# Performance work log

Hardware: AMD Instinct MI355X
Metric: run time of the kernel (lower is better)

Reference implementation:

```python
import jax, jax.numpy as jnp
import numpy as np
from jax import lax

S = 9      # patch feature size (3x3 flattened)
HID = 15   # MI-net hidden width
B = 4096
IMG = 192
PAD = 6


def _linear_params(k, fin, fout):
    bound = 1.0 / np.sqrt(fin)
    kw, kb = jax.random.split(k)
    w = jax.random.uniform(kw, (fout, fin), minval=-bound, maxval=bound, dtype=jnp.float32)
    b = jax.random.uniform(kb, (fout,), minval=-bound, maxval=bound, dtype=jnp.float32)
    return w, b


def setup_inputs() -> dict:
    key = jax.random.key(0)
    ks = jax.random.split(key, 12)
    x = jax.random.normal(ks[0], (B, 1, IMG, IMG), dtype=jnp.float32)
    hc = IMG // 3  # conv output side (stride-3 valid conv)
    ij = jax.random.randint(ks[1], (B, 2), 0, hc, dtype=jnp.int32)
    perm = jax.random.permutation(ks[2], B).astype(jnp.int32)
    cb = 1.0 / np.sqrt(1 * 3 * 3)
    conv_w = jax.random.uniform(ks[3], (1, 1, 3, 3), minval=-cb, maxval=cb, dtype=jnp.float32)
    conv_b = jax.random.uniform(ks[4], (1,), minval=-cb, maxval=cb, dtype=jnp.float32)
    xw1, xb1 = _linear_params(ks[5], S, S)
    xw2, xb2 = _linear_params(ks[6], S, S)
    xw3, xb3 = _linear_params(ks[7], S, HID)
    yw1, yb1 = _linear_params(ks[8], S, S)
    yw2, yb2 = _linear_params(ks[9], S, S)
    yw3, yb3 = _linear_params(ks[10], S, HID)
    fw, fb = _linear_params(ks[11], HID, 1)
    return dict(x=x, ij=ij, perm=perm, conv_w=conv_w, conv_b=conv_b,
                xw1=xw1, xb1=xb1, xw2=xw2, xb2=xb2, xw3=xw3, xb3=xb3,
                yw1=yw1, yb1=yb1, yw2=yw2, yb2=yb2, yw3=yw3, yb3=yb3,
                fw=fw, fb=fb)


def _mi_net(p1, p2, xw1, xb1, xw2, xb2, xw3, xb3,
            yw1, yb1, yw2, yb2, yw3, yb3, fw, fb):
    ix = p1 + jax.nn.relu(p1 @ xw1.T + xb1)
    ix = ix + jax.nn.relu(ix @ xw2.T + xb2)
    ix = ix @ xw3.T + xb3
    iy = p2 + jax.nn.relu(p2 @ yw1.T + yb1)
    iy = iy + jax.nn.relu(iy @ yw2.T + yb2)
    iy = iy @ yw3.T + yb3
    h1 = jax.nn.relu(ix + iy)
    return h1 @ fw.T + fb  # [B, 1]


def reference(x, ij, perm, conv_w, conv_b,
              xw1, xb1, xw2, xb2, xw3, xb3,
              yw1, yb1, yw2, yb2, yw3, yb3, fw, fb):
    # stride-3 valid conv: [B,1,IMG,IMG] -> [B,1,64,64]
    co = lax.conv_general_dilated(x, conv_w, (3, 3), 'VALID',
                                  dimension_numbers=('NCHW', 'OIHW', 'NCHW'))
    co = co[:, 0] + conv_b[0]  # [B, Hc, Wc]
    bn, hc, wc = co.shape
    # pad_circular(data, 6)[i:i+3, j:j+6] == data[(i-6+r) % Hc, (j-6+c) % Wc]
    rows = (ij[:, 0:1] - PAD + jnp.arange(3, dtype=jnp.int32)) % hc  # [B,3]
    cols = (ij[:, 1:2] - PAD + jnp.arange(6, dtype=jnp.int32)) % wc  # [B,6]
    rect = co[jnp.arange(bn)[:, None, None], rows[:, :, None], cols[:, None, :]]  # [B,3,6]
    patch1 = rect[:, :, :3].reshape(-1, S)
    patch2 = rect[:, :, 3:].reshape(-1, S)
    patch2_sh = patch2[perm]
    pred_xy = _mi_net(patch1, patch2, xw1, xb1, xw2, xb2, xw3, xb3,
                      yw1, yb1, yw2, yb2, yw3, yb3, fw, fb)
    pred_x_y = _mi_net(patch1, patch2_sh, xw1, xb1, xw2, xb2, xw3, xb3,
                       yw1, yb1, yw2, yb2, yw3, yb3, fw, fb)
    ret = jnp.mean(pred_xy) - jnp.log(jnp.mean(jnp.exp(pred_x_y)))
    return -ret
```

## Files before the change

kernel.cpp:

```cpp
#include <hip/hip_runtime.h>
#include <math.h>

#define BATCH 4096
#define IMGD 192
#define HC 64
#define PADV 6
#define NBLK2 256
#define IPB 16

__device__ __forceinline__ void branch9(const float* __restrict__ s, int off,
                                        const float* __restrict__ p, float* __restrict__ out)
{
    float v[9];
    #pragma unroll
    for (int j = 0; j < 9; ++j) {
        float a = s[off + 81 + j];
        #pragma unroll
        for (int k = 0; k < 9; ++k) a += p[k] * s[off + j * 9 + k];
        v[j] = p[j] + fmaxf(a, 0.0f);
    }
    float u[9];
    #pragma unroll
    for (int j = 0; j < 9; ++j) {
        float a = s[off + 171 + j];
        #pragma unroll
        for (int k = 0; k < 9; ++k) a += v[k] * s[off + 90 + j * 9 + k];
        u[j] = v[j] + fmaxf(a, 0.0f);
    }
    #pragma unroll
    for (int j = 0; j < 15; ++j) {
        float a = s[off + 315 + j];
        #pragma unroll
        for (int k = 0; k < 9; ++k) a += u[k] * s[off + 180 + j * 9 + k];
        out[j] = a;
    }
}

__global__ __launch_bounds__(256) void k_fused(
    const float* __restrict__ x, const int* __restrict__ ij,
    const int* __restrict__ perm,
    const float* __restrict__ cw, const float* __restrict__ cb,
    const float* __restrict__ xw1, const float* __restrict__ xb1,
    const float* __restrict__ xw2, const float* __restrict__ xb2,
    const float* __restrict__ xw3, const float* __restrict__ xb3,
    const float* __restrict__ yw1, const float* __restrict__ yb1,
    const float* __restrict__ yw2, const float* __restrict__ yb2,
    const float* __restrict__ yw3, const float* __restrict__ yb3,
    const float* __restrict__ fw, const float* __restrict__ fb,
    float* __restrict__ partials)
{
    __shared__ float s[676];
    __shared__ int   pidx[IPB];
    __shared__ int   ij4[IPB * 4];
    __shared__ float lpatch[IPB * 27];
    __shared__ float bout[48 * 15];

    int t  = threadIdx.x;
    int b0 = blockIdx.x * IPB;

    for (int i = t; i < 81; i += 256)  { s[i] = xw1[i];        s[330 + i] = yw1[i];
                                         s[90 + i] = xw2[i];   s[420 + i] = yw2[i]; }
    for (int i = t; i < 135; i += 256) { s[180 + i] = xw3[i];  s[510 + i] = yw3[i]; }
    if (t < 9)  { s[81 + t] = xb1[t];   s[171 + t] = xb2[t];
                  s[411 + t] = yb1[t];  s[501 + t] = yb2[t]; }
    if (t < 15) { s[315 + t] = xb3[t];  s[645 + t] = yb3[t];  s[660 + t] = fw[t]; }
    if (t == 0) s[675] = fb[0];

    float w[9];
    #pragma unroll
    for (int i = 0; i < 9; ++i) w[i] = cw[i];
    float cbias = cb[0];

    if (t < IPB) pidx[t] = perm[b0 + t];
    __syncthreads();
    if (t < 2 * IPB) {
        int item = t & (IPB - 1);
        int sel  = t >> 4;
        int bb   = sel ? pidx[item] : (b0 + item);
        ij4[item * 4 + sel * 2 + 0] = ij[2 * bb];
        ij4[item * 4 + sel * 2 + 1] = ij[2 * bb + 1];
    }
    __syncthreads();

    for (int idx = t; idx < IPB * 27; idx += 256) {
        int item = idx / 27;
        int p    = idx - item * 27;
        int r, c, sel, slot;
        if (p < 18) {
            r = p / 6;  c = p - r * 6;  sel = 0;
            int half = (c >= 3) ? 1 : 0;
            slot = half * 9 + r * 3 + (c - 3 * half);
        } else {
            int q = p - 18;
            r = q / 3;  c = 3 + (q - r * 3);  sel = 1;
            slot = 18 + q;
        }
        int bb = sel ? pidx[item] : (b0 + item);
        int i0 = ij4[item * 4 + sel * 2], j0 = ij4[item * 4 + sel * 2 + 1];
        int rr = i0 - PADV + r;  if (rr < 0) rr += HC;
        int cc = j0 - PADV + c;  if (cc < 0) cc += HC;
        const float* xp = x + (size_t)bb * (IMGD * IMGD)
                            + (size_t)(rr * 3) * IMGD + cc * 3;
        float v = cbias;
        v += xp[0]          * w[0] + xp[1]            * w[1] + xp[2]            * w[2];
        v += xp[IMGD]       * w[3] + xp[IMGD + 1]     * w[4] + xp[IMGD + 2]     * w[5];
        v += xp[2 * IMGD]   * w[6] + xp[2 * IMGD + 1] * w[7] + xp[2 * IMGD + 2] * w[8];
        lpatch[item * 27 + slot] = v;
    }
    __syncthreads();

    if (t < 48) {
        int item   = t & 15;
        int branch = t >> 4;
        int woff   = (branch == 0) ? 0 : 330;
        int pbase  = item * 27 + branch * 9;
        float p[9];
        #pragma unroll
        for (int k = 0; k < 9; ++k) p[k] = lpatch[pbase + k];
        float o[15];
        branch9(s, woff, p, o);
        #pragma unroll
        for (int j = 0; j < 15; ++j) bout[t * 15 + j] = o[j];
    }
    __syncthreads();

    if (t < IPB) {
        float fbv = s[675];
        float pxy = fbv, pxs = fbv;
        #pragma unroll
        for (int j = 0; j < 15; ++j) {
            float oxj  = bout[t * 15 + j];
            float oyj  = bout[(16 + t) * 15 + j];
            float oysj = bout[(32 + t) * 15 + j];
            float fwj  = s[660 + j];
            pxy += fmaxf(oxj + oyj,  0.0f) * fwj;
            pxs += fmaxf(oxj + oysj, 0.0f) * fwj;
        }
        float e = expf(pxs);
        #pragma unroll
        for (int o = 8; o > 0; o >>= 1) {
            pxy += __shfl_down(pxy, o);
            e   += __shfl_down(e, o);
        }
        if (t == 0) {
            partials[blockIdx.x]         = pxy;
            partials[NBLK2 + blockIdx.x] = e;
        }
    }
}

__global__ __launch_bounds__(256) void k_final(const float* __restrict__ partials,
                                               float* __restrict__ out)
{
    __shared__ float r1[4], r2[4];
    int t = threadIdx.x;
    float sx = partials[t];
    float se = partials[NBLK2 + t];
    #pragma unroll
    for (int o = 32; o > 0; o >>= 1) {
        sx += __shfl_down(sx, o);
        se += __shfl_down(se, o);
    }
    int wid = t >> 6, lane = t & 63;
    if (lane == 0) { r1[wid] = sx; r2[wid] = se; }
    __syncthreads();
    if (t == 0) {
        float S  = (r1[0] + r1[1]) + (r1[2] + r1[3]);
        float E  = (r2[0] + r2[1]) + (r2[2] + r2[3]);
        out[0] = logf(E / (float)BATCH) - S / (float)BATCH;
    }
}

extern "C" void kernel_launch(void* const* d_in, const int* in_sizes, int n_in,
                              void* d_out, int out_size, void* d_ws, size_t ws_size,
                              hipStream_t stream)
{
    const float* x    = (const float*)d_in[0];
    const int*   ij   = (const int*)d_in[1];
    const int*   perm = (const int*)d_in[2];
    const float* cw   = (const float*)d_in[3];
    const float* cb   = (const float*)d_in[4];
    const float* xw1  = (const float*)d_in[5];
    const float* xb1  = (const float*)d_in[6];
    const float* xw2  = (const float*)d_in[7];
    const float* xb2  = (const float*)d_in[8];
    const float* xw3  = (const float*)d_in[9];
    const float* xb3  = (const float*)d_in[10];
    const float* yw1  = (const float*)d_in[11];
    const float* yb1  = (const float*)d_in[12];
    const float* yw2  = (const float*)d_in[13];
    const float* yb2  = (const float*)d_in[14];
    const float* yw3  = (const float*)d_in[15];
    const float* yb3  = (const float*)d_in[16];
    const float* fw   = (const float*)d_in[17];
    const float* fb   = (const float*)d_in[18];

    float* partials = (float*)d_ws;

    k_fused<<<NBLK2, 256, 0, stream>>>(x, ij, perm, cw, cb,
                                       xw1, xb1, xw2, xb2, xw3, xb3,
                                       yw1, yb1, yw2, yb2, yw3, yb3,
                                       fw, fb, partials);
    k_final<<<1, 256, 0, stream>>>(partials, (float*)d_out);
}
```

Before: 12.38 us.

## Bulk-load ij table to LDS, remove a barrier, unroll gathers, pad weights for vector loads

Each block now copies the whole 32 KB ij table into shared memory with int4 loads, at the same time as the perm and weight loads, which removes one barrier and the dependent ij gather round trip. The conv gather loop is unrolled into two fixed slots per thread so all 18 global loads are issued before any arithmetic. Weight rows are padded to 12 floats so the MLP can read them with float4 shared loads. The MLP threads are spread across three wavefronts instead of packed into one. The cost is 32 KB of extra LDS per block and redundant global reads of ij by all 256 blocks, which may reduce occupancy.

New measurement: 12.73 us. +2.8%, slower.

```diff
diff --git a/kernel.cpp b/kernel.cpp
--- a/kernel.cpp
+++ b/kernel.cpp
@@ -8,33 +8,16 @@
 #define NBLK2 256
 #define IPB 16
 
-__device__ __forceinline__ void branch9(const float* __restrict__ s, int off,
-                                        const float* __restrict__ p, float* __restrict__ out)
-{
-    float v[9];
-    #pragma unroll
-    for (int j = 0; j < 9; ++j) {
-        float a = s[off + 81 + j];
-        #pragma unroll
-        for (int k = 0; k < 9; ++k) a += p[k] * s[off + j * 9 + k];
-        v[j] = p[j] + fmaxf(a, 0.0f);
-    }
-    float u[9];
-    #pragma unroll
-    for (int j = 0; j < 9; ++j) {
-        float a = s[off + 171 + j];
-        #pragma unroll
-        for (int k = 0; k < 9; ++k) a += v[k] * s[off + 90 + j * 9 + k];
-        u[j] = v[j] + fmaxf(a, 0.0f);
-    }
-    #pragma unroll
-    for (int j = 0; j < 15; ++j) {
-        float a = s[off + 315 + j];
-        #pragma unroll
-        for (int k = 0; k < 9; ++k) a += u[k] * s[off + 180 + j * 9 + k];
-        out[j] = a;
-    }
-}
+#define XB 0
+#define YB 432
+#define W1O 0
+#define W2O 108
+#define W3O 216
+#define B1O 396
+#define B2O 405
+#define B3O 414
+#define FWO 864
+#define FBO 879
 
 __global__ __launch_bounds__(256) void k_fused(
     const float* __restrict__ x, const int* __restrict__ ij,
@@ -49,90 +32,153 @@
     const float* __restrict__ fw, const float* __restrict__ fb,
     float* __restrict__ partials)
 {
-    __shared__ float s[676];
+    __shared__ __align__(16) float s[880];
+    __shared__ __align__(16) int   ija[BATCH * 2];
     __shared__ int   pidx[IPB];
-    __shared__ int   ij4[IPB * 4];
     __shared__ float lpatch[IPB * 27];
     __shared__ float bout[48 * 15];
 
     int t  = threadIdx.x;
     int b0 = blockIdx.x * IPB;
 
-    for (int i = t; i < 81; i += 256)  { s[i] = xw1[i];        s[330 + i] = yw1[i];
-                                         s[90 + i] = xw2[i];   s[420 + i] = yw2[i]; }
-    for (int i = t; i < 135; i += 256) { s[180 + i] = xw3[i];  s[510 + i] = yw3[i]; }
-    if (t < 9)  { s[81 + t] = xb1[t];   s[171 + t] = xb2[t];
-                  s[411 + t] = yb1[t];  s[501 + t] = yb2[t]; }
-    if (t < 15) { s[315 + t] = xb3[t];  s[645 + t] = yb3[t];  s[660 + t] = fw[t]; }
-    if (t == 0) s[675] = fb[0];
+    {
+        int4* d = (int4*)ija;
+        const int4* g = (const int4*)ij;
+        #pragma unroll
+        for (int i = 0; i < 8; ++i) d[t + 256 * i] = g[t + 256 * i];
+    }
+    if (t < IPB) pidx[t] = perm[b0 + t];
+
+    for (int i = t; i < 108; i += 256) {
+        int row = i / 12, col = i - row * 12;
+        if (col < 9) {
+            int src = row * 9 + col;
+            s[XB + W1O + i] = xw1[src];  s[XB + W2O + i] = xw2[src];
+            s[YB + W1O + i] = yw1[src];  s[YB + W2O + i] = yw2[src];
+        }
+    }
+    for (int i = t; i < 180; i += 256) {
+        int row = i / 12, col = i - row * 12;
+        if (col < 9) {
+            int src = row * 9 + col;
+            s[XB + W3O + i] = xw3[src];  s[YB + W3O + i] = yw3[src];
+        }
+    }
+    if (t >= 192) {
+        int tb = t - 192;
+        if (tb < 9)       { s[XB + B1O + tb] = xb1[tb];  s[XB + B2O + tb] = xb2[tb];
+                            s[YB + B1O + tb] = yb1[tb];  s[YB + B2O + tb] = yb2[tb]; }
+        else if (tb < 24) { int j = tb - 9;  s[XB + B3O + j] = xb3[j];  s[YB + B3O + j] = yb3[j]; }
+        else if (tb < 39) { int j = tb - 24; s[FWO + j] = fw[j]; }
+        else if (tb == 39){ s[FBO] = fb[0]; }
+    }
 
     float w[9];
     #pragma unroll
     for (int i = 0; i < 9; ++i) w[i] = cw[i];
     float cbias = cb[0];
-
-    if (t < IPB) pidx[t] = perm[b0 + t];
-    __syncthreads();
-    if (t < 2 * IPB) {
-        int item = t & (IPB - 1);
-        int sel  = t >> 4;
-        int bb   = sel ? pidx[item] : (b0 + item);
-        ij4[item * 4 + sel * 2 + 0] = ij[2 * bb];
-        ij4[item * 4 + sel * 2 + 1] = ij[2 * bb + 1];
-    }
-    __syncthreads();
-
-    for (int idx = t; idx < IPB * 27; idx += 256) {
-        int item = idx / 27;
-        int p    = idx - item * 27;
-        int r, c, sel, slot;
-        if (p < 18) {
-            r = p / 6;  c = p - r * 6;  sel = 0;
-            int half = (c >= 3) ? 1 : 0;
-            slot = half * 9 + r * 3 + (c - 3 * half);
-        } else {
-            int q = p - 18;
-            r = q / 3;  c = 3 + (q - r * 3);  sel = 1;
-            slot = 18 + q;
-        }
-        int bb = sel ? pidx[item] : (b0 + item);
-        int i0 = ij4[item * 4 + sel * 2], j0 = ij4[item * 4 + sel * 2 + 1];
-        int rr = i0 - PADV + r;  if (rr < 0) rr += HC;
-        int cc = j0 - PADV + c;  if (cc < 0) cc += HC;
-        const float* xp = x + (size_t)bb * (IMGD * IMGD)
-                            + (size_t)(rr * 3) * IMGD + cc * 3;
-        float v = cbias;
-        v += xp[0]          * w[0] + xp[1]            * w[1] + xp[2]            * w[2];
-        v += xp[IMGD]       * w[3] + xp[IMGD + 1]     * w[4] + xp[IMGD + 2]     * w[5];
-        v += xp[2 * IMGD]   * w[6] + xp[2 * IMGD + 1] * w[7] + xp[2 * IMGD + 2] * w[8];
-        lpatch[item * 27 + slot] = v;
-    }
-    __syncthreads();
-
-    if (t < 48) {
-        int item   = t & 15;
-        int branch = t >> 4;
-        int woff   = (branch == 0) ? 0 : 330;
-        int pbase  = item * 27 + branch * 9;
-        float p[9];
-        #pragma unroll
-        for (int k = 0; k < 9; ++k) p[k] = lpatch[pbase + k];
-        float o[15];
-        branch9(s, woff, p, o);
-        #pragma unroll
-        for (int j = 0; j < 15; ++j) bout[t * 15 + j] = o[j];
+    __syncthreads();
+
+    {
+        int idxA = t;
+        int itemA = idxA / 27;  int pA = idxA - itemA * 27;
+        int rA, cA, selA, slotA;
+        if (pA < 18) { rA = pA / 6; cA = pA - rA * 6; selA = 0;
+                       int h = (cA >= 3); slotA = h * 9 + rA * 3 + (cA - 3 * h); }
+        else         { int q = pA - 18; rA = q / 3; cA = 3 + q - rA * 3; selA = 1; slotA = 18 + q; }
+        int bbA = selA ? pidx[itemA] : (b0 + itemA);
+        int i0A = ija[2 * bbA], j0A = ija[2 * bbA + 1];
+        int rrA = i0A - PADV + rA;  if (rrA < 0) rrA += HC;
+        int ccA = j0A - PADV + cA;  if (ccA < 0) ccA += HC;
+        const float* pa = x + (size_t)bbA * (IMGD * IMGD) + (size_t)(rrA * 3) * IMGD + ccA * 3;
+
+        bool hasB = (t < 176);
+        int idxB = t + 256;
+        int itemB = idxB / 27;  int pB = idxB - itemB * 27;
+        int rB, cB, selB, slotB;
+        if (pB < 18) { rB = pB / 6; cB = pB - rB * 6; selB = 0;
+                       int h = (cB >= 3); slotB = h * 9 + rB * 3 + (cB - 3 * h); }
+        else         { int q = pB - 18; rB = q / 3; cB = 3 + q - rB * 3; selB = 1; slotB = 18 + q; }
+        itemB = hasB ? itemB : 0;
+        int bbB = selB ? pidx[itemB] : (b0 + itemB);
+        int i0B = ija[2 * bbB], j0B = ija[2 * bbB + 1];
+        int rrB = i0B - PADV + rB;  if (rrB < 0) rrB += HC;
+        int ccB = j0B - PADV + cB;  if (ccB < 0) ccB += HC;
+        const float* pb = hasB ? (x + (size_t)bbB * (IMGD * IMGD) + (size_t)(rrB * 3) * IMGD + ccB * 3)
+                               : pa;
+
+        float a0 = pa[0],          a1 = pa[1],            a2 = pa[2];
+        float a3 = pa[IMGD],       a4 = pa[IMGD + 1],     a5 = pa[IMGD + 2];
+        float a6 = pa[2 * IMGD],   a7 = pa[2 * IMGD + 1], a8 = pa[2 * IMGD + 2];
+        float e0 = pb[0],          e1 = pb[1],            e2 = pb[2];
+        float e3 = pb[IMGD],       e4 = pb[IMGD + 1],     e5 = pb[IMGD + 2];
+        float e6 = pb[2 * IMGD],   e7 = pb[2 * IMGD + 1], e8 = pb[2 * IMGD + 2];
+
+        float vA = cbias + a0*w[0] + a1*w[1] + a2*w[2] + a3*w[3] + a4*w[4]
+                         + a5*w[5] + a6*w[6] + a7*w[7] + a8*w[8];
+        lpatch[itemA * 27 + slotA] = vA;
+        if (hasB) {
+            float vB = cbias + e0*w[0] + e1*w[1] + e2*w[2] + e3*w[3] + e4*w[4]
+                             + e5*w[5] + e6*w[6] + e7*w[7] + e8*w[8];
+            lpatch[itemB * 27 + slotB] = vB;
+        }
+    }
+    __syncthreads();
+
+    {
+        int wv = t >> 6, l = t & 63;
+        if (wv < 3 && l < 16) {
+            int woff = (wv == 0) ? XB : YB;
+            int ib = wv * 16 + l;
+            float p[9];
+            #pragma unroll
+            for (int k = 0; k < 9; ++k) p[k] = lpatch[l * 27 + wv * 9 + k];
+
+            float v[9];
+            #pragma unroll
+            for (int j = 0; j < 9; ++j) {
+                const float4 r0 = *(const float4*)&s[woff + W1O + j * 12];
+                const float4 r1 = *(const float4*)&s[woff + W1O + j * 12 + 4];
+                float acc = s[woff + B1O + j]
+                    + r0.x*p[0] + r0.y*p[1] + r0.z*p[2] + r0.w*p[3]
+                    + r1.x*p[4] + r1.y*p[5] + r1.z*p[6] + r1.w*p[7]
+                    + s[woff + W1O + j * 12 + 8] * p[8];
+                v[j] = p[j] + fmaxf(acc, 0.0f);
+            }
+            float u[9];
+            #pragma unroll
+            for (int j = 0; j < 9; ++j) {
+                const float4 r0 = *(const float4*)&s[woff + W2O + j * 12];
+                const float4 r1 = *(const float4*)&s[woff + W2O + j * 12 + 4];
+                float acc = s[woff + B2O + j]
+                    + r0.x*v[0] + r0.y*v[1] + r0.z*v[2] + r0.w*v[3]
+                    + r1.x*v[4] + r1.y*v[5] + r1.z*v[6] + r1.w*v[7]
+                    + s[woff + W2O + j * 12 + 8] * v[8];
+                u[j] = v[j] + fmaxf(acc, 0.0f);
+            }
+            #pragma unroll
+            for (int j = 0; j < 15; ++j) {
+                const float4 r0 = *(const float4*)&s[woff + W3O + j * 12];
+                const float4 r1 = *(const float4*)&s[woff + W3O + j * 12 + 4];
+                float acc = s[woff + B3O + j]
+                    + r0.x*u[0] + r0.y*u[1] + r0.z*u[2] + r0.w*u[3]
+                    + r1.x*u[4] + r1.y*u[5] + r1.z*u[6] + r1.w*u[7]
+                    + s[woff + W3O + j * 12 + 8] * u[8];
+                bout[ib * 15 + j] = acc;
+            }
+        }
     }
     __syncthreads();
 
     if (t < IPB) {
-        float fbv = s[675];
+        float fbv = s[FBO];
         float pxy = fbv, pxs = fbv;
         #pragma unroll
         for (int j = 0; j < 15; ++j) {
             float oxj  = bout[t * 15 + j];
             float oyj  = bout[(16 + t) * 15 + j];
             float oysj = bout[(32 + t) * 15 + j];
-            float fwj  = s[660 + j];
+            float fwj  = s[FWO + j];
             pxy += fmaxf(oxj + oyj,  0.0f) * fwj;
             pxs += fmaxf(oxj + oysj, 0.0f) * fwj;
         }
@@ -165,8 +211,8 @@
     if (lane == 0) { r1[wid] = sx; r2[wid] = se; }
     __syncthreads();
     if (t == 0) {
-        float S  = (r1[0] + r1[1]) + (r1[2] + r1[3]);
-        float E  = (r2[0] + r2[1]) + (r2[2] + r2[3]);
+        float S = (r1[0] + r1[1]) + (r1[2] + r1[3]);
+        float E = (r2[0] + r2[1]) + (r2[2] + r2[3]);
         out[0] = logf(E / (float)BATCH) - S / (float)BATCH;
     }
 }
```
